# Optimization experiments

Hardware: AMD Instinct MI355X
Metric: run time of the kernel (lower is better)

## Reference

```python
import jax, jax.numpy as jnp
import numpy as np

# qshift_a: Kingsbury 10-tap Q-shift filters (sum(h0a) = sqrt(2)).
_H0A = np.array([0.0351638365171441, 0.0, -0.0883294244510729,
                 0.233890320607236, 0.760272369066126, 0.587518297723561,
                 0.0, -0.114301837144249, 0.0, 0.0], dtype=np.float64)
_H0B = _H0A[::-1].copy()
_ALT = (-1.0) ** np.arange(10)
_H1A = _H0B * _ALT            # highpass tree a
_H1B = _H1A[::-1].copy()
# synthesis filters (g0a = h0b, g0b = h0a, g1a = h1b, g1b = h1a)
G0A = _H0B.astype(np.float32)
G0B = _H0A.astype(np.float32)
G1A = _H1B.astype(np.float32)
G1B = _H1A.astype(np.float32)


def _reflect(x, minx, maxx):
    # dtcwt symmetric-extension index reflection (static, numpy)
    x = np.asarray(x, dtype=np.float64)
    rng = maxx - minx
    rng2 = 2.0 * rng
    mod = np.fmod(x - minx, rng2)
    normed = np.where(mod < 0, mod + rng2, mod)
    out = np.where(normed >= rng, rng2 - normed, normed) + minx
    return out.astype(np.int64)


def _colifilt(X, ha, hb):
    # X: (B, C, r, c) -> (B, C, 2r, c). ha, hb are 1-D numpy filters (static).
    m = ha.shape[0]
    m2 = m // 2
    assert m2 % 2 == 1, 'implemented for 10/14/18-tap qshift (m/2 odd)'
    b, ch, r, c = X.shape
    r2 = r // 2
    xe = _reflect(np.arange(-m2, r + m2), -0.5, r - 0.5)   # static indices
    t = np.arange(2, r + m - 1, 2)
    if float(np.sum(ha * hb)) > 0:
        ta, tb = t, t - 1
    else:
        ta, tb = t - 1, t
    Xa = X[:, :, xe[ta], :]   # (B, C, r/2 + m/2 - 1, c)
    Xb = X[:, :, xe[tb], :]
    hao, hae = ha[0::2], ha[1::2]
    hbo, hbe = hb[0::2], hb[1::2]

    def vconv(Z, h):
        # valid convolution along dim 2 (true conv: filter flipped)
        hf = h[::-1]
        out = Z[:, :, 0:r2, :] * float(hf[0])
        for k in range(1, m2):
            out = out + Z[:, :, k:k + r2, :] * float(hf[k])
        return out

    y = jnp.stack([vconv(Xb, hao), vconv(Xa, hbo),
                   vconv(Xb, hae), vconv(Xa, hbe)], axis=3)  # (B,C,r/2,4,c)
    return y.reshape(b, ch, 2 * r, c)


def _rowifilt(X, ha, hb):
    return jnp.swapaxes(_colifilt(jnp.swapaxes(X, 2, 3), ha, hb), 2, 3)


def _c2q(wr, wi):
    # complex pair of subbands -> real quad image. wr, wi: (B, C, 2, H, W) -> (B, C, 2H, 2W)
    w1r, w2r = wr[:, :, 0], wr[:, :, 1]
    w1i, w2i = wi[:, :, 0], wi[:, :, 1]
    x1 = w1r + w2r
    x2 = w1i + w2i
    x3 = w1i - w2i
    x4 = w2r - w1r
    b, c, h, w = x1.shape
    top = jnp.stack([x1, x2], axis=-1).reshape(b, c, h, 2 * w)
    bot = jnp.stack([x3, x4], axis=-1).reshape(b, c, h, 2 * w)
    y = jnp.stack([top, bot], axis=-2).reshape(b, c, 2 * h, 2 * w)
    return y * np.float32(1.0 / np.sqrt(2.0))


def setup_inputs() -> dict:
    key = jax.random.key(0)
    k1, k2, k3 = jax.random.split(key, 3)
    B, C, H, W = 8, 64, 128, 128
    Yl = jax.random.normal(k1, (B, C, H, W), dtype=jnp.float32)
    Yhr = jax.random.normal(k2, (B, C, 6, H // 2, W // 2), dtype=jnp.float32)
    Yhi = jax.random.normal(k3, (B, C, 6, H // 2, W // 2), dtype=jnp.float32)
    return {"Yl": Yl, "Yhr": Yhr, "Yhi": Yhi}


def reference(Yl, Yhr, Yhi):
    lh = _c2q(Yhr[:, :, 0:6:5], Yhi[:, :, 0:6:5])
    hl = _c2q(Yhr[:, :, 2:4:1], Yhi[:, :, 2:4:1])
    hh = _c2q(Yhr[:, :, 1:5:3], Yhi[:, :, 1:5:3])
    y1 = _rowifilt(Yl, G0B, G0A) + _rowifilt(hl, G1B, G1A)
    y2 = _rowifilt(lh, G0B, G0A) + _rowifilt(hh, G1B, G1A)
    return _colifilt(y1, G0B, G0A) + _colifilt(y2, G1B, G1A)
```

## Files before the change

### kernel.cpp

```cpp
#include <hip/hip_runtime.h>

#define NTHREADS 256

__device__ __forceinline__ int reflect128(int p) {
    p = (p < 0) ? (-p - 1) : p;
    p = (p >= 128) ? (255 - p) : p;
    return p;
}

__constant__ int   cs0[4] = {2, 1, 1, 0};
__constant__ int   cs1[4] = {1, 2, 0, 1};
__constant__ float cc0[4][3] = {
    { 0.760272369066126f, -0.0883294244510729f,  0.0351638365171441f},
    { 0.233890320607236f,  0.587518297723561f,  -0.114301837144249f},
    {-0.114301837144249f,  0.587518297723561f,   0.233890320607236f},
    { 0.0351638365171441f, -0.0883294244510729f, 0.760272369066126f}};
__constant__ float cc1[4][3] = {
    { 0.233890320607236f,  0.587518297723561f,  -0.114301837144249f},
    {-0.760272369066126f,  0.0883294244510729f, -0.0351638365171441f},
    {-0.0351638365171441f, 0.0883294244510729f, -0.760272369066126f},
    {-0.114301837144249f,  0.587518297723561f,   0.233890320607236f}};

__global__ __launch_bounds__(NTHREADS, 6)
void dtcwt_inv_kernel(const float* __restrict__ Yl,
                      const float* __restrict__ Yhr,
                      const float* __restrict__ Yhi,
                      float* __restrict__ out)
{
    const int tid = threadIdx.x;

    const int bid  = blockIdx.x;
    const int perx = gridDim.x >> 3;
    const int gidx = (bid & 7) * perx + (bid >> 3);
    const int plane = gidx >> 4;
    const int tile  = gidx & 15;
    const int ct = tile & 3;
    const int rt = tile >> 2;

    const int OR0 = rt * 64, OC0 = ct * 64;
    const int i0r = OR0 >> 2, i0c = OC0 >> 2;
    const int yrb = 2 * i0r - 4;
    const int icb = 2 * i0c - 4;

    const float* yl = Yl + (size_t)plane * (128 * 128);
    const float* hr = Yhr + (size_t)plane * 6 * 4096;
    const float* hi = Yhi + (size_t)plane * 6 * 4096;

    __shared__ float2 sP[40][40];
    __shared__ float2 sQ[40][40];

    const float RS2 = 0.70710678118654752440f;

    for (int e = tid; e < 1600; e += NTHREADS) {
        const int t = e / 40;
        const int u = e - t * 40;
        const int r2 = reflect128(yrb + t);
        const int c2 = reflect128(icb + u);
        sP[t][u].x = yl[r2 * 128 + c2];
    }

    for (int e = tid; e < 400; e += NTHREADS) {
        const int t2 = e / 20;
        const int u2 = e - t2 * 20;
        const int ar = i0r - 2 + t2;
        const int ac = i0c - 2 + u2;
        const int oobr = (ar < 0) | (ar >= 64);
        const int oobc = (ac < 0) | (ac >= 64);
        const int r2 = oobr ? ((ar < 0) ? (-ar - 1) : (127 - ar)) : ar;
        const int c2 = oobc ? ((ac < 0) ? (-ac - 1) : (127 - ac)) : ac;
        const int off = r2 * 64 + c2;
        const float ar0 = hr[off], ar1 = hr[4096 + off], ar2 = hr[2 * 4096 + off];
        const float ar3 = hr[3 * 4096 + off], ar4 = hr[4 * 4096 + off], ar5 = hr[5 * 4096 + off];
        const float ai0 = hi[off], ai1 = hi[4096 + off], ai2 = hi[2 * 4096 + off];
        const float ai3 = hi[3 * 4096 + off], ai4 = hi[4 * 4096 + off], ai5 = hi[5 * 4096 + off];
#pragma unroll
        for (int dt = 0; dt < 2; ++dt) {
#pragma unroll
            for (int du = 0; du < 2; ++du) {
                const int p = dt ^ oobr;
                const int q = du ^ oobc;
                const float sA = (p & q) ? -RS2 : RS2;
                const float sB = (p & (q ^ 1)) ? -RS2 : RS2;
                float b0, b5, b2v, b3, b1, b4;
                if (p == q) { b0 = ar0; b5 = ar5; b2v = ar2; b3 = ar3; b1 = ar1; b4 = ar4; }
                else        { b0 = ai0; b5 = ai5; b2v = ai2; b3 = ai3; b1 = ai1; b4 = ai4; }
                const int t = 2 * t2 + dt, u = 2 * u2 + du;
                sP[t][u].y = sA * b0 + sB * b5;
                sQ[t][u]   = make_float2(sA * b2v + sB * b3,
                                         sA * b1 + sB * b4);
            }
        }
    }
    __syncthreads();

    const int c  = tid & 63;
    const int g  = tid >> 6;
    const int jc = c & 3;
    const int q2 = c >> 2;
    const float a0  = cc0[jc][0], a1  = cc0[jc][1], a2  = cc0[jc][2];
    const float b0w = cc1[jc][0], b1w = cc1[jc][1], b2w = cc1[jc][2];
    const int ub0 = 2 * q2 + (jc & 1) + 2 * cs0[jc];
    const int ub1 = 2 * q2 + ((jc & 1) ^ 1) + 2 * cs1[jc];

    const int tb = 8 * g;
    float y1v[14], y2v[14];
#pragma unroll
    for (int k = 0; k < 14; ++k) {
        const int t = tb + 1 + k;
        const float2 P0 = sP[t][ub0], P1 = sP[t][ub0 + 2], P2 = sP[t][ub0 + 4];
        const float2 Q0 = sQ[t][ub1], Q1 = sQ[t][ub1 + 2], Q2 = sQ[t][ub1 + 4];
        y1v[k] = P0.x * a0  + P1.x * a1  + P2.x * a2
               + Q0.x * b0w + Q1.x * b1w + Q2.x * b2w;
        y2v[k] = P0.y * a0  + P1.y * a1  + P2.y * a2
               + Q0.y * b0w + Q1.y * b1w + Q2.y * b2w;
    }

    float* op = out + ((size_t)plane * 256 + OR0 + 16 * g) * 256 + OC0 + c;
#pragma unroll
    for (int j = 0; j < 4; ++j) {
        const int p0 = j & 1, p1 = p0 ^ 1;
        const int r0 = p0 + 2 * cs0[j];
        const int r1 = p1 + 2 * cs1[j];
        const float d0 = cc0[j][0], d1 = cc0[j][1], d2 = cc0[j][2];
        const float e0 = cc1[j][0], e1 = cc1[j][1], e2 = cc1[j][2];
#pragma unroll
        for (int mm = 0; mm < 4; ++mm) {
            const int k0 = 2 * mm + r0 - 1;
            const int k1 = 2 * mm + r1 - 1;
            const float acc = y1v[k0] * d0 + y1v[k0 + 2] * d1 + y1v[k0 + 4] * d2
                            + y2v[k1] * e0 + y2v[k1 + 2] * e1 + y2v[k1 + 4] * e2;
            op[(size_t)(4 * mm + j) * 256] = acc;
        }
    }
}

extern "C" void kernel_launch(void* const* d_in, const int* in_sizes, int n_in,
                              void* d_out, int out_size, void* d_ws, size_t ws_size,
                              hipStream_t stream) {
    const float* Yl  = (const float*)d_in[0];
    const float* Yhr = (const float*)d_in[1];
    const float* Yhi = (const float*)d_in[2];
    float* out = (float*)d_out;

    const int planes = in_sizes[0] / (128 * 128);
    dim3 grid(planes * 16, 1, 1);
    dtcwt_inv_kernel<<<grid, NTHREADS, 0, stream>>>(Yl, Yhr, Yhi, out);
}
```

Baseline: 259.9 us.

## Read Yl directly from global in row filter and unroll highpass staging loads

Drops the shared-memory staging of the lowpass Yl tile and reads it directly from global (via cache) inside the row-filter loop, shrinking shared memory so occupancy can rise to 8 blocks per CU. The highpass staging loop is manually unrolled into two fixed iterations with all 24 loads issued up front to increase memory-level parallelism. The trade is repeated global/L1 loads of Yl per thread (each value is read by several threads and rows) and higher register pressure under the tighter launch bound.

```diff
diff --git a/kernel.cpp b/kernel.cpp
--- a/kernel.cpp
+++ b/kernel.cpp
@@ -21,7 +21,7 @@
     {-0.0351638365171441f, 0.0883294244510729f, -0.760272369066126f},
     {-0.114301837144249f,  0.587518297723561f,   0.233890320607236f}};
 
-__global__ __launch_bounds__(NTHREADS, 6)
+__global__ __launch_bounds__(NTHREADS, 8)
 void dtcwt_inv_kernel(const float* __restrict__ Yl,
                       const float* __restrict__ Yhr,
                       const float* __restrict__ Yhi,
@@ -46,48 +46,64 @@
     const float* hr = Yhr + (size_t)plane * 6 * 4096;
     const float* hi = Yhi + (size_t)plane * 6 * 4096;
 
-    __shared__ float2 sP[40][40];
+    __shared__ float  sLh[40][40];
     __shared__ float2 sQ[40][40];
 
     const float RS2 = 0.70710678118654752440f;
 
-    for (int e = tid; e < 1600; e += NTHREADS) {
-        const int t = e / 40;
-        const int u = e - t * 40;
-        const int r2 = reflect128(yrb + t);
-        const int c2 = reflect128(icb + u);
-        sP[t][u].x = yl[r2 * 128 + c2];
-    }
+    {
+        const int e0 = tid;
+        const int e1 = tid + NTHREADS;
+        const int has1 = (e1 < 400);
 
-    for (int e = tid; e < 400; e += NTHREADS) {
-        const int t2 = e / 20;
-        const int u2 = e - t2 * 20;
-        const int ar = i0r - 2 + t2;
-        const int ac = i0c - 2 + u2;
-        const int oobr = (ar < 0) | (ar >= 64);
-        const int oobc = (ac < 0) | (ac >= 64);
-        const int r2 = oobr ? ((ar < 0) ? (-ar - 1) : (127 - ar)) : ar;
-        const int c2 = oobc ? ((ac < 0) ? (-ac - 1) : (127 - ac)) : ac;
-        const int off = r2 * 64 + c2;
-        const float ar0 = hr[off], ar1 = hr[4096 + off], ar2 = hr[2 * 4096 + off];
-        const float ar3 = hr[3 * 4096 + off], ar4 = hr[4 * 4096 + off], ar5 = hr[5 * 4096 + off];
-        const float ai0 = hi[off], ai1 = hi[4096 + off], ai2 = hi[2 * 4096 + off];
-        const float ai3 = hi[3 * 4096 + off], ai4 = hi[4 * 4096 + off], ai5 = hi[5 * 4096 + off];
+        const int t2a = e0 / 20, u2a = e0 - t2a * 20;
+        const int ara = i0r - 2 + t2a, aca = i0c - 2 + u2a;
+        const int oobra = (ara < 0) | (ara >= 64);
+        const int oobca = (aca < 0) | (aca >= 64);
+        const int r2a = oobra ? ((ara < 0) ? (-ara - 1) : (127 - ara)) : ara;
+        const int c2a = oobca ? ((aca < 0) ? (-aca - 1) : (127 - aca)) : aca;
+        const int offa = r2a * 64 + c2a;
+
+        const int e1c = has1 ? e1 : 0;
+        const int t2b = e1c / 20, u2b = e1c - t2b * 20;
+        const int arb = i0r - 2 + t2b, acb = i0c - 2 + u2b;
+        const int oobrb = (arb < 0) | (arb >= 64);
+        const int oobcb = (acb < 0) | (acb >= 64);
+        const int r2b = oobrb ? ((arb < 0) ? (-arb - 1) : (127 - arb)) : arb;
+        const int c2b = oobcb ? ((acb < 0) ? (-acb - 1) : (127 - acb)) : acb;
+        const int offb = r2b * 64 + c2b;
+
+        float Ra[6], Ia[6], Rb[6], Ib[6];
 #pragma unroll
-        for (int dt = 0; dt < 2; ++dt) {
+        for (int k = 0; k < 6; ++k) { Ra[k] = hr[k * 4096 + offa]; Ia[k] = hi[k * 4096 + offa]; }
 #pragma unroll
-            for (int du = 0; du < 2; ++du) {
-                const int p = dt ^ oobr;
-                const int q = du ^ oobc;
-                const float sA = (p & q) ? -RS2 : RS2;
-                const float sB = (p & (q ^ 1)) ? -RS2 : RS2;
-                float b0, b5, b2v, b3, b1, b4;
-                if (p == q) { b0 = ar0; b5 = ar5; b2v = ar2; b3 = ar3; b1 = ar1; b4 = ar4; }
-                else        { b0 = ai0; b5 = ai5; b2v = ai2; b3 = ai3; b1 = ai1; b4 = ai4; }
-                const int t = 2 * t2 + dt, u = 2 * u2 + du;
-                sP[t][u].y = sA * b0 + sB * b5;
-                sQ[t][u]   = make_float2(sA * b2v + sB * b3,
-                                         sA * b1 + sB * b4);
+        for (int k = 0; k < 6; ++k) { Rb[k] = hr[k * 4096 + offb]; Ib[k] = hi[k * 4096 + offb]; }
+
+#pragma unroll
+        for (int wq = 0; wq < 2; ++wq) {
+            if (wq == 1 && !has1) break;
+            const float* R = (wq == 0) ? Ra : Rb;
+            const float* I = (wq == 0) ? Ia : Ib;
+            const int t2 = (wq == 0) ? t2a : t2b;
+            const int u2 = (wq == 0) ? u2a : u2b;
+            const int oobr = (wq == 0) ? oobra : oobrb;
+            const int oobc = (wq == 0) ? oobca : oobcb;
+#pragma unroll
+            for (int dt = 0; dt < 2; ++dt) {
+#pragma unroll
+                for (int du = 0; du < 2; ++du) {
+                    const int p = dt ^ oobr;
+                    const int q = du ^ oobc;
+                    const float sA = (p & q) ? -RS2 : RS2;
+                    const float sB = (p & (q ^ 1)) ? -RS2 : RS2;
+                    float b0, b5, b2v, b3, b1, b4;
+                    if (p == q) { b0 = R[0]; b5 = R[5]; b2v = R[2]; b3 = R[3]; b1 = R[1]; b4 = R[4]; }
+                    else        { b0 = I[0]; b5 = I[5]; b2v = I[2]; b3 = I[3]; b1 = I[1]; b4 = I[4]; }
+                    const int t = 2 * t2 + dt, u = 2 * u2 + du;
+                    sLh[t][u] = sA * b0 + sB * b5;
+                    sQ[t][u]  = make_float2(sA * b2v + sB * b3,
+                                            sA * b1 + sB * b4);
+                }
             }
         }
     }
@@ -101,18 +117,22 @@
     const float b0w = cc1[jc][0], b1w = cc1[jc][1], b2w = cc1[jc][2];
     const int ub0 = 2 * q2 + (jc & 1) + 2 * cs0[jc];
     const int ub1 = 2 * q2 + ((jc & 1) ^ 1) + 2 * cs1[jc];
+    const int ic0 = reflect128(icb + ub0);
+    const int ic1 = reflect128(icb + ub0 + 2);
+    const int ic2 = reflect128(icb + ub0 + 4);
 
     const int tb = 8 * g;
     float y1v[14], y2v[14];
 #pragma unroll
     for (int k = 0; k < 14; ++k) {
         const int t = tb + 1 + k;
-        const float2 P0 = sP[t][ub0], P1 = sP[t][ub0 + 2], P2 = sP[t][ub0 + 4];
+        const int ry = reflect128(yrb + t);
+        const float* yrow = yl + ry * 128;
         const float2 Q0 = sQ[t][ub1], Q1 = sQ[t][ub1 + 2], Q2 = sQ[t][ub1 + 4];
-        y1v[k] = P0.x * a0  + P1.x * a1  + P2.x * a2
-               + Q0.x * b0w + Q1.x * b1w + Q2.x * b2w;
-        y2v[k] = P0.y * a0  + P1.y * a1  + P2.y * a2
-               + Q0.y * b0w + Q1.y * b1w + Q2.y * b2w;
+        y1v[k] = yrow[ic0]   * a0  + yrow[ic1]       * a1  + yrow[ic2]       * a2
+               + Q0.x        * b0w + Q1.x            * b1w + Q2.x            * b2w;
+        y2v[k] = sLh[t][ub0] * a0  + sLh[t][ub0 + 2] * a1  + sLh[t][ub0 + 4] * a2
+               + Q0.y        * b0w + Q1.y            * b1w + Q2.y            * b2w;
     }
 
     float* op = out + ((size_t)plane * 256 + OR0 + 16 * g) * 256 + OC0 + c;
```

New measurement: 486.6 us. 87.2% more time.
